# Performance work log

Hardware: AMD Instinct MI355X
Metric: run time of the kernel (lower is better)

The kernel has to match this reference:

```python
import jax, jax.numpy as jnp
import numpy as np

CONF_THRESH = 0.01
TOP_K = 200
NMS_THRESH = 0.45


def setup_inputs() -> dict:
    key = jax.random.key(0)
    k1, k2, k3, k4, k5 = jax.random.split(key, 5)
    B, N, C = 32, 8732, 21
    return {
        "loc_data": jax.random.normal(k1, (B, N, 4), jnp.float32),
        "conf_data": jax.random.normal(k2, (B, N, C), jnp.float32),
        "pose_data": jax.random.normal(k3, (B, N, 32), jnp.float32),
        "line_data": jax.random.normal(k4, (B, N, 3), jnp.float32),
        "dbox_list": jax.random.uniform(k5, (N, 4), jnp.float32),
    }


def decode(loc, dbox):
    # loc, dbox: [N,4]; variances 0.1 / 0.2 as in the torch decode()
    cxcy = dbox[:, :2] + loc[:, :2] * 0.1 * dbox[:, 2:]
    wh = dbox[:, 2:] * jnp.exp(loc[:, 2:] * 0.2)
    mins = cxcy - wh / 2.0
    maxs = mins + wh
    return jnp.concatenate([mins, maxs], axis=1)  # [N,4] xyxy


def nms_class(boxes, scores, poses, lines):
    """Greedy NMS for one (batch, class). boxes [N,4], scores [N] (softmax probs).
    Matches torch nm_suppression: candidates are the top_k by score above
    conf_thresh; suppress IoU > overlap; at most top_k kept."""
    s0 = jnp.where(scores > CONF_THRESH, scores, -jnp.inf)
    _, cand_idx = jax.lax.top_k(s0, TOP_K)  # descending-score candidate pool
    cb = boxes[cand_idx]                     # [K,4]
    cs = s0[cand_idx]                        # [K], -inf where below threshold
    x1, y1, x2, y2 = cb[:, 0], cb[:, 1], cb[:, 2], cb[:, 3]
    area = (x2 - x1) * (y2 - y1)
    K = TOP_K
    ar = jnp.arange(K)

    def step(s, _):
        i = jnp.argmax(s)
        take = jnp.isfinite(s[i])
        xx1 = jnp.maximum(x1, x1[i])
        yy1 = jnp.maximum(y1, y1[i])
        xx2 = jnp.minimum(x2, x2[i])
        yy2 = jnp.minimum(y2, y2[i])
        inter = jnp.clip(xx2 - xx1, 0.0) * jnp.clip(yy2 - yy1, 0.0)
        union = area - inter + area[i]
        iou = inter / union
        supp = (iou > NMS_THRESH) | (ar == i)
        s_new = jnp.where(take & supp, -jnp.inf, s)
        return s_new, (i, take)

    _, (pos, take) = jax.lax.scan(step, cs, None, length=K)
    gi = cand_idx[pos]  # global box indices of kept detections [K]
    row = jnp.concatenate(
        [scores[gi][:, None], boxes[gi], poses[gi], lines[gi]], axis=1
    )  # [K, 1+4+32+3] = [200, 40]
    return row * take[:, None].astype(row.dtype)


def reference(loc_data, conf_data, pose_data, line_data, dbox_list):
    conf = jax.nn.softmax(conf_data, axis=-1)                       # [B,N,C]
    boxes = jax.vmap(decode, in_axes=(0, None))(loc_data, dbox_list)  # [B,N,4]
    per_cls = jax.vmap(nms_class, in_axes=(None, 1, None, None))    # over classes
    per_batch = jax.vmap(per_cls, in_axes=(0, 0, 0, 0))             # over batch
    out = per_batch(boxes, conf, pose_data, line_data)              # [B,C,200,40]
    return out.at[:, 0].set(0.0)  # class 0 (background) is skipped in torch loop
```

## Files before the change

### kernel.cpp

```cpp
#include <hip/hip_runtime.h>
#include <math.h>

#define BB 32
#define NN 8732
#define CC 21
#define TOPK 200
#define NPOSE 32
#define NLINE 3
#define NBINS 2048
#define CAP 4096
#define ROWW 40

__device__ inline void softmax_es(const float* __restrict__ p, float* e, float& sumOut) {
  float m = p[0];
#pragma unroll
  for (int c = 1; c < CC; ++c) m = fmaxf(m, p[c]);
#pragma unroll
  for (int c = 0; c < CC; ++c) e[c] = (float)exp((double)(p[c] - m));
  float r0 = e[0] + e[8], r1 = e[1] + e[9], r2 = e[2] + e[10], r3 = e[3] + e[11];
  float r4 = e[4] + e[12], r5 = e[5] + e[13], r6 = e[6] + e[14], r7 = e[7] + e[15];
  float res = ((r0 + r1) + (r2 + r3)) + ((r4 + r5) + (r6 + r7));
  res += e[16]; res += e[17]; res += e[18]; res += e[19]; res += e[20];
  sumOut = res;
}

__global__ __launch_bounds__(256) void score_kernel(
    const float* __restrict__ conf, float* __restrict__ scores) {
  int i = blockIdx.x * 256 + threadIdx.x;
  if (i >= BB * NN) return;
  int b = i / NN, n = i - b * NN;
  const float* p = conf + (size_t)i * CC;
  float e[CC], sum;
  softmax_es(p, e, sum);
#pragma unroll
  for (int c = 0; c < CC; ++c)
    scores[((size_t)b * CC + c) * NN + n] = e[c] / sum;
}

__global__ __launch_bounds__(256) void aux_kernel(
    const float* __restrict__ conf, float2* __restrict__ aux) {
  int i = blockIdx.x * 256 + threadIdx.x;
  if (i >= BB * NN) return;
  const float* p = conf + (size_t)i * CC;
  float e[CC], sum;
  softmax_es(p, e, sum);
  float m = p[0];
#pragma unroll
  for (int c = 1; c < CC; ++c) m = fmaxf(m, p[c]);
  aux[i] = make_float2(m, sum);
}

__global__ __launch_bounds__(256) void nms_kernel(
    const float* __restrict__ loc, const float* __restrict__ conf,
    const float* __restrict__ pose, const float* __restrict__ line,
    const float* __restrict__ dbox, const float* __restrict__ scores,
    const float2* __restrict__ aux, int mode, float* __restrict__ out) {
  const int bc = blockIdx.x;
  const int b = bc / CC, c = bc - b * CC;
  const int tid = threadIdx.x;
  float* outSlab = out + (size_t)bc * (TOPK * ROWW);

  {
    float4 z = make_float4(0.f, 0.f, 0.f, 0.f);
    float4* o4 = (float4*)outSlab;
    for (int i = tid; i < TOPK * ROWW / 4; i += 256) o4[i] = z;
  }
  if (c == 0) return;

  __shared__ int hist[NBINS];
  __shared__ int chunkSum[256];
  __shared__ float cscore[CAP];
  __shared__ int cidx[CAP];
  __shared__ float bx1[TOPK], by1[TOPK], bx2[TOPK], by2[TOPK], barea[TOPK];
  __shared__ int alive[TOPK], kept[TOPK];
  __shared__ int sBT, sCnt, sKept;

  for (int i = tid; i < NBINS; i += 256) hist[i] = 0;
  if (tid == 0) { sCnt = 0; sKept = 0; }
  __syncthreads();

  const float* scoresB = scores + ((size_t)b * CC + c) * NN;
  const float2* auxB = aux + (size_t)b * NN;
  const float* confB = conf + (size_t)b * NN * CC + c;

  for (int n = tid; n < NN; n += 256) {
    float s;
    if (mode == 2) {
      s = scoresB[n];
    } else if (mode == 1) {
      float2 a = auxB[n];
      s = (float)exp((double)(confB[(size_t)n * CC] - a.x)) / a.y;
    } else {
      const float* p = conf + ((size_t)b * NN + n) * CC;
      float e[CC], sum;
      softmax_es(p, e, sum);
      s = e[c] / sum;
    }
    if (s > 0.01f) {
      unsigned u = __float_as_uint(s);
      int bin = (int)(u >> 15) - 30720;
      bin = bin < 0 ? 0 : (bin > NBINS - 1 ? NBINS - 1 : bin);
      atomicAdd(&hist[bin], 1);
    }
  }
  __syncthreads();

  {
    int s8 = 0;
#pragma unroll
    for (int k = 0; k < 8; ++k) s8 += hist[tid * 8 + k];
    chunkSum[tid] = s8;
  }
  __syncthreads();
  if (tid == 0) {
    int cum = 0, bt = 0;
    for (int ch = 255; ch >= 0; --ch) {
      if (cum + chunkSum[ch] >= TOPK) {
        for (int bin = ch * 8 + 7;; --bin) {
          cum += hist[bin];
          if (cum >= TOPK || bin == ch * 8) { bt = bin; break; }
        }
        break;
      }
      cum += chunkSum[ch];
    }
    sBT = bt;
  }
  __syncthreads();
  const int bt = sBT;

  for (int n = tid; n < NN; n += 256) {
    float s;
    if (mode == 2) {
      s = scoresB[n];
    } else if (mode == 1) {
      float2 a = auxB[n];
      s = (float)exp((double)(confB[(size_t)n * CC] - a.x)) / a.y;
    } else {
      const float* p = conf + ((size_t)b * NN + n) * CC;
      float e[CC], sum;
      softmax_es(p, e, sum);
      s = e[c] / sum;
    }
    if (s > 0.01f) {
      unsigned u = __float_as_uint(s);
      int bin = (int)(u >> 15) - 30720;
      bin = bin < 0 ? 0 : (bin > NBINS - 1 ? NBINS - 1 : bin);
      if (bin >= bt) {
        int p = atomicAdd(&sCnt, 1);
        if (p < CAP) { cscore[p] = s; cidx[p] = n; }
      }
    }
  }
  __syncthreads();
  const int M = sCnt < CAP ? sCnt : CAP;
  if (M == 0) return;

  int P = 1;
  while (P < M) P <<= 1;
  for (int i = M + tid; i < P; i += 256) {
    cscore[i] = -1e30f;
    cidx[i] = 0x7fffffff;
  }
  __syncthreads();
  for (int k = 2; k <= P; k <<= 1) {
    for (int j = k >> 1; j > 0; j >>= 1) {
      for (int i = tid; i < P; i += 256) {
        int ixj = i ^ j;
        if (ixj > i) {
          float si = cscore[i], sj = cscore[ixj];
          int ii = cidx[i], ij = cidx[ixj];
          bool agt = (si > sj) || (si == sj && ii < ij);
          bool up = ((i & k) == 0);
          if (up ? !agt : agt) {
            cscore[i] = sj; cscore[ixj] = si;
            cidx[i] = ij;  cidx[ixj] = ii;
          }
        }
      }
      __syncthreads();
    }
  }

  const int K = M < TOPK ? M : TOPK;

  const float* locB = loc + (size_t)b * NN * 4;
  for (int t = tid; t < K; t += 256) {
    int n = cidx[t];
    float l0 = locB[(size_t)n * 4 + 0], l1 = locB[(size_t)n * 4 + 1];
    float l2 = locB[(size_t)n * 4 + 2], l3 = locB[(size_t)n * 4 + 3];
    float d0 = dbox[(size_t)n * 4 + 0], d1 = dbox[(size_t)n * 4 + 1];
    float d2 = dbox[(size_t)n * 4 + 2], d3 = dbox[(size_t)n * 4 + 3];
    float cx = d0 + (l0 * 0.1f) * d2;
    float cy = d1 + (l1 * 0.1f) * d3;
    float w = d2 * (float)exp((double)(l2 * 0.2f));
    float h = d3 * (float)exp((double)(l3 * 0.2f));
    float x1 = cx - w * 0.5f;
    float y1 = cy - h * 0.5f;
    float x2 = x1 + w;
    float y2 = y1 + h;
    bx1[t] = x1; by1[t] = y1; bx2[t] = x2; by2[t] = y2;
    barea[t] = (x2 - x1) * (y2 - y1);
    alive[t] = 1;
  }
  __syncthreads();

  for (int j = 0; j < K; ++j) {
    __syncthreads();
    if (!alive[j]) continue;
    if (tid == 0) kept[sKept++] = j;
    float x1j = bx1[j], y1j = by1[j], x2j = bx2[j], y2j = by2[j], aj = barea[j];
    for (int l = j + 1 + tid; l < K; l += 256) {
      if (!alive[l]) continue;
      float xx1 = fmaxf(bx1[l], x1j);
      float yy1 = fmaxf(by1[l], y1j);
      float xx2 = fminf(bx2[l], x2j);
      float yy2 = fminf(by2[l], y2j);
      float iw = fmaxf(xx2 - xx1, 0.0f);
      float ih = fmaxf(yy2 - yy1, 0.0f);
      float inter = iw * ih;
      float uni = (barea[l] - inter) + aj;
      if (inter / uni > 0.45f) alive[l] = 0;
    }
  }
  __syncthreads();

  const int nk = sKept;
  const float* poseB = pose + (size_t)b * NN * NPOSE;
  const float* lineB = line + (size_t)b * NN * NLINE;
  for (int t = tid; t < nk; t += 256) {
    int j = kept[t];
    int n = cidx[j];
    float* row = outSlab + (size_t)t * ROWW;
    row[0] = cscore[j];
    row[1] = bx1[j];
    row[2] = by1[j];
    row[3] = bx2[j];
    row[4] = by2[j];
#pragma unroll
    for (int q = 0; q < NPOSE; ++q) row[5 + q] = poseB[(size_t)n * NPOSE + q];
    row[37] = lineB[(size_t)n * NLINE + 0];
    row[38] = lineB[(size_t)n * NLINE + 1];
    row[39] = lineB[(size_t)n * NLINE + 2];
  }
}

extern "C" void kernel_launch(void* const* d_in, const int* in_sizes, int n_in,
                              void* d_out, int out_size, void* d_ws, size_t ws_size,
                              hipStream_t stream) {
  const float* loc  = (const float*)d_in[0];
  const float* conf = (const float*)d_in[1];
  const float* pose = (const float*)d_in[2];
  const float* line = (const float*)d_in[3];
  const float* dbox = (const float*)d_in[4];
  float* out = (float*)d_out;

  const size_t scoreBytes = (size_t)BB * CC * NN * sizeof(float);
  const size_t auxBytes   = (size_t)BB * NN * sizeof(float2);

  int mode;
  float* scores = nullptr;
  float2* aux = nullptr;
  if (ws_size >= scoreBytes) {
    mode = 2; scores = (float*)d_ws;
  } else if (ws_size >= auxBytes) {
    mode = 1; aux = (float2*)d_ws;
  } else {
    mode = 0;
  }

  const int total = BB * NN;
  if (mode == 2) {
    score_kernel<<<(total + 255) / 256, 256, 0, stream>>>(conf, scores);
  } else if (mode == 1) {
    aux_kernel<<<(total + 255) / 256, 256, 0, stream>>>(conf, aux);
  }
  nms_kernel<<<BB * CC, 256, 0, stream>>>(loc, conf, pose, line, dbox,
                                          scores, aux, mode, out);
}
```

Baseline: 197.4 us.

## Run NMS in one wavefront with registers, inline double exp, stage softmax loads in LDS

The greedy NMS loop, which needed a block-wide barrier per candidate, now runs inside a single 64-lane wavefront. Box data and alive bits sit in registers, the selected box is broadcast with shuffles, and the kept list is built with ballot/popcount. The library double exp is replaced by an inlined polynomial fexp. The score kernel stages its conf reads through shared memory so the global loads are coalesced, and CAP drops to 1024 to cut LDS use and raise occupancy. The risks are overflow of the smaller candidate buffer when many scores tie in the threshold bin, and slight numerical differences from the custom exp.

```diff
diff --git a/kernel.cpp b/kernel.cpp
--- a/kernel.cpp
+++ b/kernel.cpp
@@ -8,15 +8,39 @@
 #define NPOSE 32
 #define NLINE 3
 #define NBINS 2048
-#define CAP 4096
+#define CAP 1024
 #define ROWW 40
 
-__device__ inline void softmax_es(const float* __restrict__ p, float* e, float& sumOut) {
+__device__ __forceinline__ double fexp(double x) {
+  const double LOG2E = 1.4426950408889634074;
+  const double LN2HI = 6.93147180369123816490e-01;
+  const double LN2LO = 1.90821492927058770002e-10;
+  double kd = rint(x * LOG2E);
+  double r = fma(-kd, LN2HI, x);
+  r = fma(-kd, LN2LO, r);
+  double p = 2.08767569878680989792e-09;
+  p = fma(p, r, 2.50521083854417187751e-08);
+  p = fma(p, r, 2.75573192239858906526e-07);
+  p = fma(p, r, 2.75573192239858925110e-06);
+  p = fma(p, r, 2.48015873015873015873e-05);
+  p = fma(p, r, 1.98412698412698412698e-04);
+  p = fma(p, r, 1.38888888888888888889e-03);
+  p = fma(p, r, 8.33333333333333333333e-03);
+  p = fma(p, r, 4.16666666666666666667e-02);
+  p = fma(p, r, 1.66666666666666666667e-01);
+  p = fma(p, r, 0.5);
+  p = fma(p, r, 1.0);
+  p = fma(p, r, 1.0);
+  return ldexp(p, (int)kd);
+}
+
+__device__ __forceinline__ void softmax_es(const float* __restrict__ p, float* e,
+                                           float& sumOut) {
   float m = p[0];
 #pragma unroll
   for (int c = 1; c < CC; ++c) m = fmaxf(m, p[c]);
 #pragma unroll
-  for (int c = 0; c < CC; ++c) e[c] = (float)exp((double)(p[c] - m));
+  for (int c = 0; c < CC; ++c) e[c] = (float)fexp((double)(p[c] - m));
   float r0 = e[0] + e[8], r1 = e[1] + e[9], r2 = e[2] + e[10], r3 = e[3] + e[11];
   float r4 = e[4] + e[12], r5 = e[5] + e[13], r6 = e[6] + e[14], r7 = e[7] + e[15];
   float res = ((r0 + r1) + (r2 + r3)) + ((r4 + r5) + (r6 + r7));
@@ -26,12 +50,20 @@
 
 __global__ __launch_bounds__(256) void score_kernel(
     const float* __restrict__ conf, float* __restrict__ scores) {
-  int i = blockIdx.x * 256 + threadIdx.x;
+  __shared__ float buf[256 * CC];
+  const int tid = threadIdx.x;
+  const int i0 = blockIdx.x * 256;
+  const int base = i0 * CC;
+  int total = BB * NN * CC - base;
+  if (total > 256 * CC) total = 256 * CC;
+  for (int t = tid; t < total; t += 256) buf[t] = conf[base + t];
+  __syncthreads();
+  const int i = i0 + tid;
   if (i >= BB * NN) return;
-  int b = i / NN, n = i - b * NN;
-  const float* p = conf + (size_t)i * CC;
+  const float* p = buf + tid * CC;
   float e[CC], sum;
   softmax_es(p, e, sum);
+  const int b = i / NN, n = i - b * NN;
 #pragma unroll
   for (int c = 0; c < CC; ++c)
     scores[((size_t)b * CC + c) * NN + n] = e[c] / sum;
@@ -72,11 +104,11 @@
   __shared__ float cscore[CAP];
   __shared__ int cidx[CAP];
   __shared__ float bx1[TOPK], by1[TOPK], bx2[TOPK], by2[TOPK], barea[TOPK];
-  __shared__ int alive[TOPK], kept[TOPK];
+  __shared__ int kept[TOPK];
   __shared__ int sBT, sCnt, sKept;
 
   for (int i = tid; i < NBINS; i += 256) hist[i] = 0;
-  if (tid == 0) { sCnt = 0; sKept = 0; }
+  if (tid == 0) sCnt = 0;
   __syncthreads();
 
   const float* scoresB = scores + ((size_t)b * CC + c) * NN;
@@ -89,7 +121,7 @@
       s = scoresB[n];
     } else if (mode == 1) {
       float2 a = auxB[n];
-      s = (float)exp((double)(confB[(size_t)n * CC] - a.x)) / a.y;
+      s = (float)fexp((double)(confB[(size_t)n * CC] - a.x)) / a.y;
     } else {
       const float* p = conf + ((size_t)b * NN + n) * CC;
       float e[CC], sum;
@@ -135,7 +167,7 @@
       s = scoresB[n];
     } else if (mode == 1) {
       float2 a = auxB[n];
-      s = (float)exp((double)(confB[(size_t)n * CC] - a.x)) / a.y;
+      s = (float)fexp((double)(confB[(size_t)n * CC] - a.x)) / a.y;
     } else {
       const float* p = conf + ((size_t)b * NN + n) * CC;
       float e[CC], sum;
@@ -193,35 +225,73 @@
     float d2 = dbox[(size_t)n * 4 + 2], d3 = dbox[(size_t)n * 4 + 3];
     float cx = d0 + (l0 * 0.1f) * d2;
     float cy = d1 + (l1 * 0.1f) * d3;
-    float w = d2 * (float)exp((double)(l2 * 0.2f));
-    float h = d3 * (float)exp((double)(l3 * 0.2f));
+    float w = d2 * (float)fexp((double)(l2 * 0.2f));
+    float h = d3 * (float)fexp((double)(l3 * 0.2f));
     float x1 = cx - w * 0.5f;
     float y1 = cy - h * 0.5f;
     float x2 = x1 + w;
     float y2 = y1 + h;
     bx1[t] = x1; by1[t] = y1; bx2[t] = x2; by2[t] = y2;
     barea[t] = (x2 - x1) * (y2 - y1);
-    alive[t] = 1;
-  }
-  __syncthreads();
-
-  for (int j = 0; j < K; ++j) {
-    __syncthreads();
-    if (!alive[j]) continue;
-    if (tid == 0) kept[sKept++] = j;
-    float x1j = bx1[j], y1j = by1[j], x2j = bx2[j], y2j = by2[j], aj = barea[j];
-    for (int l = j + 1 + tid; l < K; l += 256) {
-      if (!alive[l]) continue;
-      float xx1 = fmaxf(bx1[l], x1j);
-      float yy1 = fmaxf(by1[l], y1j);
-      float xx2 = fminf(bx2[l], x2j);
-      float yy2 = fminf(by2[l], y2j);
-      float iw = fmaxf(xx2 - xx1, 0.0f);
-      float ih = fmaxf(yy2 - yy1, 0.0f);
-      float inter = iw * ih;
-      float uni = (barea[l] - inter) + aj;
-      if (inter / uni > 0.45f) alive[l] = 0;
-    }
+  }
+  __syncthreads();
+
+  if (tid < 64) {
+    const int lane = tid;
+    float X1[4], Y1[4], X2[4], Y2[4], AR[4];
+    unsigned aliveBits = 0;
+#pragma unroll
+    for (int s = 0; s < 4; ++s) {
+      int l = s * 64 + lane;
+      if (l < K) {
+        X1[s] = bx1[l]; Y1[s] = by1[l]; X2[s] = bx2[l]; Y2[s] = by2[l];
+        AR[s] = barea[l];
+        aliveBits |= 1u << s;
+      } else {
+        X1[s] = 0.f; Y1[s] = 0.f; X2[s] = 0.f; Y2[s] = 0.f; AR[s] = 0.f;
+      }
+    }
+#pragma unroll
+    for (int s = 0; s < 4; ++s) {
+      int jmax = K - s * 64;
+      if (jmax > 64) jmax = 64;
+      for (int jj = 0; jj < jmax; ++jj) {
+        unsigned abits = (unsigned)__shfl((int)aliveBits, jj, 64);
+        if (!((abits >> s) & 1)) continue;
+        const int j = s * 64 + jj;
+        float x1j = __shfl(X1[s], jj, 64);
+        float y1j = __shfl(Y1[s], jj, 64);
+        float x2j = __shfl(X2[s], jj, 64);
+        float y2j = __shfl(Y2[s], jj, 64);
+        float aj  = __shfl(AR[s], jj, 64);
+#pragma unroll
+        for (int t2 = 0; t2 < 4; ++t2) {
+          int l = t2 * 64 + lane;
+          if (((aliveBits >> t2) & 1) && l > j) {
+            float xx1 = fmaxf(X1[t2], x1j);
+            float yy1 = fmaxf(Y1[t2], y1j);
+            float xx2 = fminf(X2[t2], x2j);
+            float yy2 = fminf(Y2[t2], y2j);
+            float iw = fmaxf(xx2 - xx1, 0.0f);
+            float ih = fmaxf(yy2 - yy1, 0.0f);
+            float inter = iw * ih;
+            float uni = (AR[t2] - inter) + aj;
+            if (inter / uni > 0.45f) aliveBits &= ~(1u << t2);
+          }
+        }
+      }
+    }
+    int base2 = 0;
+#pragma unroll
+    for (int s = 0; s < 4; ++s) {
+      unsigned long long mb = __ballot((int)((aliveBits >> s) & 1));
+      if ((aliveBits >> s) & 1) {
+        int rank = base2 + __popcll(mb & ((1ull << lane) - 1));
+        kept[rank] = s * 64 + lane;
+      }
+      base2 += __popcll(mb);
+    }
+    if (lane == 0) sKept = base2;
   }
   __syncthreads();
 
```

New measurement: 204.3 us. 1.04x slower.
